# Optimization experiments

Measured on AMD Instinct MI355X. Metric: run time of the kernel, lower is better.

## Reference

```python
import jax, jax.numpy as jnp
import numpy as np

B, S, D = 4, 2048, 768
H = 12
HD = D // H  # 64
SCALE = HD ** -0.5

def setup_inputs() -> dict:
    key = jax.random.key(0)
    k1, k2, k3 = jax.random.split(key, 3)
    x = jax.random.normal(k1, (B, S, D), dtype=jnp.float32)
    w_qkv = jax.random.normal(k2, (D, 3 * D), dtype=jnp.float32) * (D ** -0.5)
    w_out = jax.random.normal(k3, (D, D), dtype=jnp.float32) * (D ** -0.5)
    b_out = jnp.zeros((D,), dtype=jnp.float32)
    return {"x": x, "w_qkv": w_qkv, "w_out": w_out, "b_out": b_out}

def reference(x, w_qkv, w_out, b_out):
    B_, S_, D_ = x.shape
    # qkv projection (no bias), then 'b s (qkv h d) -> qkv b h s d'
    qkv = (x @ w_qkv).reshape(B_, S_, 3, H, HD).transpose(2, 0, 3, 1, 4)
    q, k, v = qkv[0], qkv[1], qkv[2]  # each [B, H, S, HD]
    att = jnp.einsum('bhxd,bhyd->bhxy', q, k) * SCALE
    att = jax.nn.softmax(att, axis=-1)  # dropout_rate=0 -> identity
    out = jnp.einsum('bhxy,bhyd->bhxd', att, v)
    out = out.transpose(0, 2, 1, 3).reshape(B_, S_, D_)  # 'b h s d -> b s (h d)'
    return out @ w_out + b_out
```

## Files before the change

kernel.cpp:

```cpp
#include <hip/hip_runtime.h>

#define BB 4
#define SS 2048
#define DD 768
#define HH 12
#define HDIM 64

using bf16_t = __bf16;
typedef __bf16 bf16x8 __attribute__((ext_vector_type(8)));
typedef __bf16 bf16x4 __attribute__((ext_vector_type(4)));
typedef float f32x4 __attribute__((ext_vector_type(4)));
typedef unsigned int u32;

static __device__ __forceinline__ void cp16(void* lds, const void* g) {
  __builtin_amdgcn_global_load_lds(
      (const __attribute__((address_space(1))) u32*)g,
      (__attribute__((address_space(3))) u32*)lds, 16, 0, 0);
}

__global__ void cvt_x(const float* __restrict__ in, bf16_t* __restrict__ out) {
  const size_t i = ((size_t)blockIdx.x * 256 + threadIdx.x) * 8;
  f32x4 f0 = *(const f32x4*)(in + i);
  f32x4 f1 = *(const f32x4*)(in + i + 4);
  bf16x8 v;
#pragma unroll
  for (int j = 0; j < 4; j++) { v[j] = (bf16_t)f0[j]; v[4 + j] = (bf16_t)f1[j]; }
  *(bf16x8*)(out + i) = v;
}

__global__ void wt_transpose(const float* __restrict__ in, bf16_t* __restrict__ out,
                             int K, int N) {
  __shared__ bf16_t tile[64][65];
  const int n0 = blockIdx.x * 64, k0 = blockIdx.y * 64;
  const int t = threadIdx.x;
  const int r = t >> 2;
  const int c0 = (t & 3) * 16;
  const float* src = in + (size_t)(k0 + r) * N + n0 + c0;
#pragma unroll
  for (int q = 0; q < 4; q++) {
    f32x4 f = *(const f32x4*)(src + q * 4);
#pragma unroll
    for (int j = 0; j < 4; j++) tile[r][c0 + q * 4 + j] = (bf16_t)f[j];
  }
  __syncthreads();
  bf16x8 o0, o1;
#pragma unroll
  for (int j = 0; j < 8; j++) { o0[j] = tile[c0 + j][r]; o1[j] = tile[c0 + 8 + j][r]; }
  *(bf16x8*)(out + (size_t)(n0 + r) * K + k0 + c0) = o0;
  *(bf16x8*)(out + (size_t)(n0 + r) * K + k0 + c0 + 8) = o1;
}

template <int MODE>
__global__ __launch_bounds__(256, 4)
void gemm_bt(const bf16_t* __restrict__ A, const bf16_t* __restrict__ Bt,
             int M, int N, int K,
             bf16_t* __restrict__ q_out, bf16_t* __restrict__ k_out,
             bf16_t* __restrict__ vt_out,
             float* __restrict__ Cout, const float* __restrict__ bias) {
  __shared__ bf16_t As[128][64];
  __shared__ bf16_t Bs[128][64];
  const int t = threadIdx.x;
  const int lane = t & 63, wave = t >> 6;
  const int l15 = lane & 15, quad = lane >> 4;
  const int wm = (wave >> 1) * 64, wn = (wave & 1) * 64;
  const int m0 = blockIdx.y * 128, n0 = blockIdx.x * 128;
  const int srow = lane >> 3;
  const int schunk = ((lane & 7) ^ srow) * 8;
  const int rsw = l15 & 7;

  f32x4 acc[4][4];
#pragma unroll
  for (int i = 0; i < 4; i++)
#pragma unroll
    for (int j = 0; j < 4; j++) acc[i][j] = (f32x4){0.f, 0.f, 0.f, 0.f};

  for (int k0 = 0; k0 < K; k0 += 64) {
    __syncthreads();
#pragma unroll
    for (int p = 0; p < 4; p++) {
      const int row = wave * 32 + p * 8 + srow;
      const bf16_t* asrc;
      if (MODE == 0) {
        asrc = A + (size_t)(m0 + row) * K + k0 + schunk;
      } else {
        const int mm = m0 + row, b = mm >> 11, s = mm & 2047, h = k0 >> 6;
        asrc = A + (((size_t)(b * HH + h)) * SS + s) * HDIM + schunk;
      }
      cp16(&As[wave * 32 + p * 8][0], asrc);
      cp16(&Bs[wave * 32 + p * 8][0],
           Bt + (size_t)(n0 + row) * K + k0 + schunk);
    }
    __syncthreads();
#pragma unroll
    for (int kk = 0; kk < 2; kk++) {
      bf16x8 af[4], bfr[4];
#pragma unroll
      for (int i = 0; i < 4; i++)
        af[i] = *(const bf16x8*)&As[wm + i * 16 + l15][((kk * 4 + quad) ^ rsw) * 8];
#pragma unroll
      for (int j = 0; j < 4; j++)
        bfr[j] = *(const bf16x8*)&Bs[wn + j * 16 + l15][((kk * 4 + quad) ^ rsw) * 8];
#pragma unroll
      for (int i = 0; i < 4; i++)
#pragma unroll
        for (int j = 0; j < 4; j++)
          acc[i][j] = __builtin_amdgcn_mfma_f32_16x16x32_bf16(af[i], bfr[j], acc[i][j], 0, 0, 0);
    }
  }

#pragma unroll
  for (int i = 0; i < 4; i++) {
    const int mbase = m0 + wm + i * 16 + quad * 4;
#pragma unroll
    for (int j = 0; j < 4; j++) {
      const int n = n0 + wn + j * 16 + l15;
#pragma unroll
      for (int r = 0; r < 4; r++) {
        const float v = acc[i][j][r];
        const int mm = mbase + r;
        if (MODE == 0) {
          const int sel = n / DD;
          const int rem = n - sel * DD;
          const int h = rem >> 6, d = rem & 63;
          const int b = mm >> 11, s = mm & 2047;
          const bf16_t bv = (bf16_t)v;
          if (sel == 2) {
            const int sp = (s & ~63) | (((s & 15) << 2) | ((s >> 4) & 3));
            vt_out[((size_t)(b * HH + h) * HDIM + d) * SS + sp] = bv;
          } else {
            const size_t idx = (((size_t)(b * HH + h)) * SS + s) * HDIM + d;
            if (sel == 0) q_out[idx] = bv; else k_out[idx] = bv;
          }
        } else {
          Cout[(size_t)mm * N + n] = v + bias[n];
        }
      }
    }
  }
}

__global__ __launch_bounds__(256, 4)
void attn_kernel(bf16_t* __restrict__ Qio, const bf16_t* __restrict__ Kg,
                 const bf16_t* __restrict__ Vt) {
  __shared__ bf16_t Ks[64][72];
  __shared__ bf16_t Vts[64][72];
  __shared__ bf16_t Ps[128][72];
  const int t = threadIdx.x;
  const int lane = t & 63, wave = t >> 6;
  const int l15 = lane & 15, quad = lane >> 4;
  const int bh = blockIdx.y;
  const int q0 = blockIdx.x * 128;
  const size_t base = (size_t)bh * SS * HDIM;
  const size_t baset = (size_t)bh * HDIM * SS;
  const int wq = wave * 32;
  const int sr = t >> 3, sc = (t & 7) * 8;

  bf16x8 qf[2][2];
#pragma unroll
  for (int rt = 0; rt < 2; rt++)
#pragma unroll
    for (int kh = 0; kh < 2; kh++)
      qf[rt][kh] = *(const bf16x8*)(Qio + base + (size_t)(q0 + wq + rt * 16 + l15) * HDIM +
                                    kh * 32 + quad * 8);

  float l_loc[2][4];
  f32x4 o_acc[2][4];
#pragma unroll
  for (int rt = 0; rt < 2; rt++) {
#pragma unroll
    for (int r = 0; r < 4; r++) l_loc[rt][r] = 0.f;
#pragma unroll
    for (int dt = 0; dt < 4; dt++) o_acc[rt][dt] = (f32x4){0.f, 0.f, 0.f, 0.f};
  }
  const float cs = 0.125f * 1.44269504088896340736f;

  for (int k0 = 0; k0 < SS; k0 += 64) {
    __syncthreads();
#pragma unroll
    for (int p = 0; p < 2; p++) {
      const int r = p * 32 + sr;
      *(bf16x8*)&Ks[r][sc] = *(const bf16x8*)(Kg + base + (size_t)(k0 + r) * HDIM + sc);
      *(bf16x8*)&Vts[r][sc] = *(const bf16x8*)(Vt + baset + (size_t)r * SS + k0 + sc);
    }
    __syncthreads();

    f32x4 s_acc[2][4];
#pragma unroll
    for (int rt = 0; rt < 2; rt++)
#pragma unroll
      for (int ct = 0; ct < 4; ct++) s_acc[rt][ct] = (f32x4){0.f, 0.f, 0.f, 0.f};
#pragma unroll
    for (int kh = 0; kh < 2; kh++) {
#pragma unroll
      for (int ct = 0; ct < 4; ct++) {
        bf16x8 kf = *(const bf16x8*)&Ks[ct * 16 + l15][kh * 32 + quad * 8];
#pragma unroll
        for (int rt = 0; rt < 2; rt++)
          s_acc[rt][ct] = __builtin_amdgcn_mfma_f32_16x16x32_bf16(qf[rt][kh], kf, s_acc[rt][ct], 0, 0, 0);
      }
    }

#pragma unroll
    for (int rt = 0; rt < 2; rt++) {
#pragma unroll
      for (int r = 0; r < 4; r++) {
        const float p0 = exp2f(s_acc[rt][0][r] * cs);
        const float p1 = exp2f(s_acc[rt][1][r] * cs);
        const float p2 = exp2f(s_acc[rt][2][r] * cs);
        const float p3 = exp2f(s_acc[rt][3][r] * cs);
        l_loc[rt][r] += (p0 + p1) + (p2 + p3);
        bf16x4 pk = {(bf16_t)p0, (bf16_t)p1, (bf16_t)p2, (bf16_t)p3};
        *(bf16x4*)&Ps[wq + rt * 16 + quad * 4 + r][l15 * 4] = pk;
      }
    }

    __syncthreads();

#pragma unroll
    for (int kh = 0; kh < 2; kh++) {
      bf16x8 pf[2];
#pragma unroll
      for (int rt = 0; rt < 2; rt++)
        pf[rt] = *(const bf16x8*)&Ps[wq + rt * 16 + l15][kh * 32 + quad * 8];
#pragma unroll
      for (int dt = 0; dt < 4; dt++) {
        bf16x8 vf = *(const bf16x8*)&Vts[dt * 16 + l15][kh * 32 + quad * 8];
#pragma unroll
        for (int rt = 0; rt < 2; rt++)
          o_acc[rt][dt] = __builtin_amdgcn_mfma_f32_16x16x32_bf16(pf[rt], vf, o_acc[rt][dt], 0, 0, 0);
      }
    }
  }

#pragma unroll
  for (int rt = 0; rt < 2; rt++) {
#pragma unroll
    for (int r = 0; r < 4; r++) {
      float l = l_loc[rt][r];
#pragma unroll
      for (int off = 1; off < 16; off <<= 1) l += __shfl_xor(l, off);
      const float inv = 1.0f / l;
      const int s = q0 + wq + rt * 16 + quad * 4 + r;
#pragma unroll
      for (int dt = 0; dt < 4; dt++) {
        const int d = dt * 16 + l15;
        Qio[base + (size_t)s * HDIM + d] = (bf16_t)(o_acc[rt][dt][r] * inv);
      }
    }
  }
}

extern "C" void kernel_launch(void* const* d_in, const int* in_sizes, int n_in,
                              void* d_out, int out_size, void* d_ws, size_t ws_size,
                              hipStream_t stream) {
  const float* x = (const float*)d_in[0];
  const float* w_qkv = (const float*)d_in[1];
  const float* w_out = (const float*)d_in[2];
  const float* b_out = (const float*)d_in[3];
  float* out = (float*)d_out;

  char* ws = (char*)d_ws;
  bf16_t* wqkv_t = (bf16_t*)ws; ws += (size_t)3 * DD * DD * 2;
  bf16_t* wout_t = (bf16_t*)ws; ws += (size_t)DD * DD * 2;
  bf16_t* q_ws = (bf16_t*)ws;   ws += (size_t)BB * HH * SS * HDIM * 2;
  bf16_t* k_ws = (bf16_t*)ws;
  bf16_t* vt_sc = (bf16_t*)d_out;
  bf16_t* xb = (bf16_t*)d_out + (size_t)BB * SS * DD;

  cvt_x<<<(BB * SS * DD) / (256 * 8), 256, 0, stream>>>(x, xb);
  wt_transpose<<<dim3(3 * DD / 64, DD / 64), 256, 0, stream>>>(w_qkv, wqkv_t, DD, 3 * DD);
  wt_transpose<<<dim3(DD / 64, DD / 64), 256, 0, stream>>>(w_out, wout_t, DD, DD);
  gemm_bt<0><<<dim3(3 * DD / 128, BB * SS / 128), 256, 0, stream>>>(
      xb, wqkv_t, BB * SS, 3 * DD, DD, q_ws, k_ws, vt_sc, nullptr, nullptr);
  attn_kernel<<<dim3(SS / 128, BB * HH), 256, 0, stream>>>(q_ws, k_ws, vt_sc);
  gemm_bt<1><<<dim3(DD / 128, BB * SS / 128), 256, 0, stream>>>(
      q_ws, wout_t, BB * SS, DD, DD, nullptr, nullptr, nullptr, out, b_out);
}
```

Baseline: 272.1 us.

## Double-buffer K/V tiles with async LDS loads, swizzle LDS, prescale Q

```diff
diff --git a/kernel.cpp b/kernel.cpp
--- a/kernel.cpp
+++ b/kernel.cpp
@@ -108,6 +108,7 @@
     }
   }
 
+  const float QSCALE = 0.125f * 1.44269504088896340736f;
 #pragma unroll
   for (int i = 0; i < 4; i++) {
     const int mbase = m0 + wm + i * 16 + quad * 4;
@@ -123,13 +124,13 @@
           const int rem = n - sel * DD;
           const int h = rem >> 6, d = rem & 63;
           const int b = mm >> 11, s = mm & 2047;
-          const bf16_t bv = (bf16_t)v;
           if (sel == 2) {
             const int sp = (s & ~63) | (((s & 15) << 2) | ((s >> 4) & 3));
-            vt_out[((size_t)(b * HH + h) * HDIM + d) * SS + sp] = bv;
+            vt_out[((size_t)(b * HH + h) * HDIM + d) * SS + sp] = (bf16_t)v;
           } else {
             const size_t idx = (((size_t)(b * HH + h)) * SS + s) * HDIM + d;
-            if (sel == 0) q_out[idx] = bv; else k_out[idx] = bv;
+            if (sel == 0) q_out[idx] = (bf16_t)(v * QSCALE);
+            else k_out[idx] = (bf16_t)v;
           }
         } else {
           Cout[(size_t)mm * N + n] = v + bias[n];
@@ -139,12 +140,12 @@
   }
 }
 
-__global__ __launch_bounds__(256, 4)
+__global__ __launch_bounds__(256, 3)
 void attn_kernel(bf16_t* __restrict__ Qio, const bf16_t* __restrict__ Kg,
                  const bf16_t* __restrict__ Vt) {
-  __shared__ bf16_t Ks[64][72];
-  __shared__ bf16_t Vts[64][72];
-  __shared__ bf16_t Ps[128][72];
+  __shared__ bf16_t Ks[2][64][64];
+  __shared__ bf16_t Vts[2][64][64];
+  __shared__ bf16_t Ps[128][64];
   const int t = threadIdx.x;
   const int lane = t & 63, wave = t >> 6;
   const int l15 = lane & 15, quad = lane >> 4;
@@ -153,7 +154,9 @@
   const size_t base = (size_t)bh * SS * HDIM;
   const size_t baset = (size_t)bh * HDIM * SS;
   const int wq = wave * 32;
-  const int sr = t >> 3, sc = (t & 7) * 8;
+  const int srow = lane >> 3;
+  const int schunk = ((lane & 7) ^ srow) * 8;
+  const int rsw = l15 & 7;
 
   bf16x8 qf[2][2];
 #pragma unroll
@@ -172,16 +175,22 @@
 #pragma unroll
     for (int dt = 0; dt < 4; dt++) o_acc[rt][dt] = (f32x4){0.f, 0.f, 0.f, 0.f};
   }
-  const float cs = 0.125f * 1.44269504088896340736f;
-
-  for (int k0 = 0; k0 < SS; k0 += 64) {
-    __syncthreads();
+
+  auto stage = [&](int k0, int buf) {
 #pragma unroll
     for (int p = 0; p < 2; p++) {
-      const int r = p * 32 + sr;
-      *(bf16x8*)&Ks[r][sc] = *(const bf16x8*)(Kg + base + (size_t)(k0 + r) * HDIM + sc);
-      *(bf16x8*)&Vts[r][sc] = *(const bf16x8*)(Vt + baset + (size_t)r * SS + k0 + sc);
-    }
+      const int row = wave * 16 + p * 8 + srow;
+      cp16(&Ks[buf][wave * 16 + p * 8][0],
+           Kg + base + (size_t)(k0 + row) * HDIM + schunk);
+      cp16(&Vts[buf][wave * 16 + p * 8][0],
+           Vt + baset + (size_t)row * SS + k0 + schunk);
+    }
+  };
+
+  stage(0, 0);
+
+  for (int it = 0; it < SS / 64; it++) {
+    const int buf = it & 1;
     __syncthreads();
 
     f32x4 s_acc[2][4];
@@ -193,7 +202,7 @@
     for (int kh = 0; kh < 2; kh++) {
 #pragma unroll
       for (int ct = 0; ct < 4; ct++) {
-        bf16x8 kf = *(const bf16x8*)&Ks[ct * 16 + l15][kh * 32 + quad * 8];
+        bf16x8 kf = *(const bf16x8*)&Ks[buf][ct * 16 + l15][((kh * 4 + quad) ^ rsw) * 8];
 #pragma unroll
         for (int rt = 0; rt < 2; rt++)
           s_acc[rt][ct] = __builtin_amdgcn_mfma_f32_16x16x32_bf16(qf[rt][kh], kf, s_acc[rt][ct], 0, 0, 0);
@@ -204,27 +213,30 @@
     for (int rt = 0; rt < 2; rt++) {
 #pragma unroll
       for (int r = 0; r < 4; r++) {
-        const float p0 = exp2f(s_acc[rt][0][r] * cs);
-        const float p1 = exp2f(s_acc[rt][1][r] * cs);
-        const float p2 = exp2f(s_acc[rt][2][r] * cs);
-        const float p3 = exp2f(s_acc[rt][3][r] * cs);
+        const float p0 = __builtin_amdgcn_exp2f(s_acc[rt][0][r]);
+        const float p1 = __builtin_amdgcn_exp2f(s_acc[rt][1][r]);
+        const float p2 = __builtin_amdgcn_exp2f(s_acc[rt][2][r]);
+        const float p3 = __builtin_amdgcn_exp2f(s_acc[rt][3][r]);
         l_loc[rt][r] += (p0 + p1) + (p2 + p3);
         bf16x4 pk = {(bf16_t)p0, (bf16_t)p1, (bf16_t)p2, (bf16_t)p3};
-        *(bf16x4*)&Ps[wq + rt * 16 + quad * 4 + r][l15 * 4] = pk;
-      }
-    }
-
-    __syncthreads();
+        const int row = wq + rt * 16 + quad * 4 + r;
+        *(bf16x4*)&Ps[row][((l15 >> 1) ^ (row & 7)) * 8 + (l15 & 1) * 4] = pk;
+      }
+    }
+
+    __syncthreads();
+
+    if (it + 1 < SS / 64) stage((it + 1) * 64, buf ^ 1);
 
 #pragma unroll
     for (int kh = 0; kh < 2; kh++) {
       bf16x8 pf[2];
 #pragma unroll
       for (int rt = 0; rt < 2; rt++)
-        pf[rt] = *(const bf16x8*)&Ps[wq + rt * 16 + l15][kh * 32 + quad * 8];
+        pf[rt] = *(const bf16x8*)&Ps[wq + rt * 16 + l15][((kh * 4 + quad) ^ rsw) * 8];
 #pragma unroll
       for (int dt = 0; dt < 4; dt++) {
-        bf16x8 vf = *(const bf16x8*)&Vts[dt * 16 + l15][kh * 32 + quad * 8];
+        bf16x8 vf = *(const bf16x8*)&Vts[buf][dt * 16 + l15][((kh * 4 + quad) ^ rsw) * 8];
 #pragma unroll
         for (int rt = 0; rt < 2; rt++)
           o_acc[rt][dt] = __builtin_amdgcn_mfma_f32_16x16x32_bf16(pf[rt], vf, o_acc[rt][dt], 0, 0, 0);
```

Result: faster. 224.9 us (-17.4%).
